# Performance work log

Hardware: AMD Instinct MI355X
Metric: run time of the kernel (lower is better)

## Reference

```python
import jax, jax.numpy as jnp
import numpy as np

HEADS = 4
DIM_HEAD = 32


def setup_inputs() -> dict:
    key = jax.random.key(0)
    k1, k2, k3, k4 = jax.random.split(key, 4)
    dim = 256
    hidden = HEADS * DIM_HEAD  # 128
    x = jax.random.normal(k1, (4, dim, 64, 64), dtype=jnp.float32)
    # 1x1 convs are channel-mixing matmuls; store weights as [out_ch, in_ch]
    w_qkv = jax.random.normal(k2, (3 * hidden, dim), dtype=jnp.float32) * (dim ** -0.5)
    w_out = jax.random.normal(k3, (dim, hidden), dtype=jnp.float32) * (hidden ** -0.5)
    b_out = jax.random.normal(k4, (dim,), dtype=jnp.float32) * 0.02
    return {"x": x, "w_qkv": w_qkv, "w_out": w_out, "b_out": b_out}


def reference(x, w_qkv, w_out, b_out):
    b, c, h, w = x.shape
    n = h * w
    scale = DIM_HEAD ** -0.5
    xf = x.reshape(b, c, n)                                   # b c n
    qkv = jnp.einsum('oc,bcn->bon', w_qkv, xf)                # b (3*H*D) n
    q, k, v = jnp.split(qkv, 3, axis=1)                       # each b (H*D) n
    q = q.reshape(b, HEADS, DIM_HEAD, n) * scale              # b h d n
    k = k.reshape(b, HEADS, DIM_HEAD, n)
    v = v.reshape(b, HEADS, DIM_HEAD, n)
    sim = jnp.einsum('bhdi,bhdj->bhij', q, k)                 # b h n n
    attn = jax.nn.softmax(sim, axis=-1)                       # stable max-subtract inside
    out = jnp.einsum('bhij,bhdj->bhdi', attn, v)              # b h d n
    out = out.reshape(b, HEADS * DIM_HEAD, n)                 # b (h d) n
    out = jnp.einsum('oc,bcn->bon', w_out, out) + b_out[None, :, None]
    return out.reshape(b, -1, h, w)
```

## Files before the change

kernel.cpp:

```cpp
#include <hip/hip_runtime.h>
#include <hip/hip_bf16.h>
#include <stdint.h>

#define B_SZ 4
#define C_IN 256
#define N_SP 4096
#define HEADS 4
#define DH 32
#define HID 128

#define BI 128
#define BJ 64
#define PP 68

typedef short short4v __attribute__((ext_vector_type(4)));
typedef short short8 __attribute__((ext_vector_type(8)));
typedef float f32x4 __attribute__((ext_vector_type(4)));

#if __has_builtin(__builtin_amdgcn_exp2f)
#define EXP2 __builtin_amdgcn_exp2f
#else
#define EXP2 exp2f
#endif

__device__ __forceinline__ short f2bfs(float f) {
  return (short)((__float_as_uint(f) + 0x8000u) >> 16);
}
__device__ __forceinline__ float bfs2f(short s) {
  return __uint_as_float(((uint32_t)(unsigned short)s) << 16);
}
__device__ __forceinline__ uint32_t pk_bf(float a, float b) {
  uint32_t ua = __float_as_uint(a) + 0x8000u;
  uint32_t ub = __float_as_uint(b) + 0x8000u;
  return (ua >> 16) | (ub & 0xffff0000u);
}
__device__ __forceinline__ short8 ld_frag(const short* p) {
  short4v a = *(const short4v*)p;
  short4v b = *(const short4v*)(p + 4);
  return __builtin_shufflevector(a, b, 0, 1, 2, 3, 4, 5, 6, 7);
}
__device__ __forceinline__ f32x4 mfma16(short8 a, short8 b, f32x4 c) {
  return __builtin_amdgcn_mfma_f32_16x16x32_bf16(a, b, c, 0, 0, 0);
}

__global__ __launch_bounds__(256) void prep_k(
    const float* __restrict__ x, const float* __restrict__ w_qkv,
    const float* __restrict__ w_out,
    short* __restrict__ xh, short* __restrict__ xl,
    short* __restrict__ wqh, short* __restrict__ wql,
    short* __restrict__ woh, short* __restrict__ wol) {
  const int t = threadIdx.x;
  const int bx = blockIdx.x;
  if (bx < 256) {
    __shared__ float T[64 * 65];
    const int b = bx >> 6, n0 = (bx & 63) * 64;
    const float* xb = x + (size_t)b * C_IN * N_SP;
    for (int c0 = 0; c0 < C_IN; c0 += 64) {
      {
        const int n = t & 63, cw = t >> 6;
#pragma unroll
        for (int i = 0; i < 16; ++i) {
          const int c = cw * 16 + i;
          T[n * 65 + c] = xb[(size_t)(c0 + c) * N_SP + n0 + n];
        }
      }
      __syncthreads();
      {
        const int n = t >> 2, cg = t & 3;
#pragma unroll
        for (int j = 0; j < 2; ++j) {
          const int c = cg * 16 + j * 8;
          short8 hv, lv;
#pragma unroll
          for (int e = 0; e < 8; ++e) {
            const float v = T[n * 65 + c + e];
            const short hh = f2bfs(v);
            hv[e] = hh;
            lv[e] = f2bfs(v - bfs2f(hh));
          }
          const size_t off = ((size_t)(b * N_SP + n0 + n)) * C_IN + c0 + c;
          *(short8*)(xh + off) = hv;
          *(short8*)(xl + off) = lv;
        }
      }
      __syncthreads();
    }
  } else {
    const int f0 = (bx - 256) * 8192;
#pragma unroll
    for (int j = 0; j < 32; ++j) {
      const int f = f0 + j * 256 + t;
      float v;
      short *dh, *dl;
      int idx;
      if (f < 384 * 256) { v = w_qkv[f]; dh = wqh; dl = wql; idx = f; }
      else { idx = f - 384 * 256; v = w_out[idx]; dh = woh; dl = wol; }
      const short hh = f2bfs(v);
      dh[idx] = hh;
      dl[idx] = f2bfs(v - bfs2f(hh));
    }
  }
}

__global__ __launch_bounds__(256) void qkv_mfma_k(
    const short* __restrict__ xh, const short* __restrict__ xl,
    const short* __restrict__ wqh, const short* __restrict__ wql,
    short* __restrict__ qt, short* __restrict__ kt, short* __restrict__ vt) {
  const int t = threadIdx.x;
  const int lane = t & 63, w = t >> 6;
  const int l15 = lane & 15, quad = lane >> 4;
  const int osec = blockIdx.y, b = blockIdx.z;
  const int n0 = blockIdx.x * 64 + w * 16;
  const size_t xrow = ((size_t)(b * N_SP + n0 + l15)) * C_IN;
  const size_t wrow = ((size_t)(osec * 128 + l15)) * C_IN;
  const bool isv = (osec == 2);
  const f32x4 zz = {0.f, 0.f, 0.f, 0.f};
  f32x4 acc[8];
#pragma unroll
  for (int ot = 0; ot < 8; ++ot) acc[ot] = zz;

  for (int k0 = 0; k0 < C_IN; k0 += 32) {
    const int ko = k0 + quad * 8;
    const short8 xhf = *(const short8*)(xh + xrow + ko);
    const short8 xlf = *(const short8*)(xl + xrow + ko);
#pragma unroll
    for (int ot = 0; ot < 8; ++ot) {
      const size_t wo = wrow + (size_t)ot * 16 * C_IN + ko;
      const short8 whf = *(const short8*)(wqh + wo);
      const short8 wlf = *(const short8*)(wql + wo);
      if (isv) {
        acc[ot] = mfma16(xhf, whf, acc[ot]);
        acc[ot] = mfma16(xlf, whf, acc[ot]);
        acc[ot] = mfma16(xhf, wlf, acc[ot]);
      } else {
        acc[ot] = mfma16(whf, xhf, acc[ot]);
        acc[ot] = mfma16(whf, xlf, acc[ot]);
        acc[ot] = mfma16(wlf, xhf, acc[ot]);
      }
    }
  }

  if (!isv) {
    const float sc = osec ? 1.f : (0.17677669529663687f * 1.4426950408889634f);
    short* dst = osec ? kt : qt;
    const int n = n0 + l15;
#pragma unroll
    for (int ot = 0; ot < 8; ++ot) {
      const int ol = ot * 16 + quad * 4;
      const int h = ol >> 5, d0 = ol & 31;
      short4v p;
#pragma unroll
      for (int r = 0; r < 4; ++r) p[r] = f2bfs(acc[ot][r] * sc);
      *(short4v*)(dst + ((size_t)(b * HEADS + h) * N_SP + n) * DH + d0) = p;
    }
  } else {
    const int n = n0 + quad * 4;
#pragma unroll
    for (int ot = 0; ot < 8; ++ot) {
      const int ol = ot * 16 + l15;
      const int h = ol >> 5, d = ol & 31;
      short4v p;
#pragma unroll
      for (int r = 0; r < 4; ++r) p[r] = f2bfs(acc[ot][r]);
      *(short4v*)(vt + ((size_t)(b * HEADS + h) * DH + d) * N_SP + n) = p;
    }
  }
}

__global__ __launch_bounds__(256, 2) void attn_k(
    const short* __restrict__ qt, const short* __restrict__ kt,
    const short* __restrict__ vt, short* __restrict__ ath,
    short* __restrict__ atl) {
  __shared__ short Ps[BI * PP];
  __shared__ float Osh[DH * 132];
  const int t = threadIdx.x;
  const int lane = t & 63, w = t >> 6;
  const int l15 = lane & 15, quad = lane >> 4;
  const int i0 = blockIdx.x * BI;
  const int bh = blockIdx.y;
  const short* qg = qt + ((size_t)bh * N_SP + i0) * DH;
  const short* kg = kt + (size_t)bh * N_SP * DH;
  const short* vg = vt + (size_t)bh * DH * N_SP;

  short8 bq[2];
#pragma unroll
  for (int tt = 0; tt < 2; ++tt)
    bq[tt] = *(const short8*)(qg + (size_t)(w * 32 + tt * 16 + l15) * DH + quad * 8);

  const f32x4 zz = {0.f, 0.f, 0.f, 0.f};
  f32x4 o_acc[2][2] = {{zz, zz}, {zz, zz}};
  float lsum[2] = {0.f, 0.f};
  short* prow[2];
#pragma unroll
  for (int tt = 0; tt < 2; ++tt) prow[tt] = Ps + (w * 32 + tt * 16 + l15) * PP;

  short8 akA[4], akB[4], vbA[2][2], vbB[2][2];
#pragma unroll
  for (int jt = 0; jt < 4; ++jt)
    akA[jt] = *(const short8*)(kg + (size_t)(jt * 16 + l15) * DH + quad * 8);
#pragma unroll
  for (int dt = 0; dt < 2; ++dt)
#pragma unroll
    for (int kk = 0; kk < 2; ++kk)
      vbA[dt][kk] = *(const short8*)(vg + (size_t)(dt * 16 + l15) * N_SP + kk * 32 + quad * 8);

  auto body = [&](const short8 (&akc)[4], const short8 (&vbc)[2][2],
                  short8 (&akn)[4], short8 (&vbn)[2][2], int jn) {
    f32x4 sf[2][4];
#pragma unroll
    for (int tt = 0; tt < 2; ++tt)
#pragma unroll
      for (int jt = 0; jt < 4; ++jt) sf[tt][jt] = mfma16(akc[jt], bq[tt], zz);
#pragma unroll
    for (int jt = 0; jt < 4; ++jt)
      akn[jt] = *(const short8*)(kg + (size_t)(jn + jt * 16 + l15) * DH + quad * 8);
#pragma unroll
    for (int dt = 0; dt < 2; ++dt)
#pragma unroll
      for (int kk = 0; kk < 2; ++kk)
        vbn[dt][kk] = *(const short8*)(vg + (size_t)(dt * 16 + l15) * N_SP + jn + kk * 32 + quad * 8);
#pragma unroll
    for (int tt = 0; tt < 2; ++tt)
#pragma unroll
      for (int jt = 0; jt < 4; ++jt) {
        const float e0 = EXP2(sf[tt][jt][0]);
        const float e1 = EXP2(sf[tt][jt][1]);
        const float e2 = EXP2(sf[tt][jt][2]);
        const float e3 = EXP2(sf[tt][jt][3]);
        lsum[tt] += (e0 + e1) + (e2 + e3);
        uint2 pk; pk.x = pk_bf(e0, e1); pk.y = pk_bf(e2, e3);
        *(uint2*)(prow[tt] + jt * 16 + quad * 4) = pk;
      }
    asm volatile("s_waitcnt lgkmcnt(0)" ::: "memory");
    short8 pa[2][2];
#pragma unroll
    for (int tt = 0; tt < 2; ++tt)
#pragma unroll
      for (int kk = 0; kk < 2; ++kk) pa[tt][kk] = ld_frag(prow[tt] + kk * 32 + quad * 8);
#pragma unroll
    for (int tt = 0; tt < 2; ++tt)
#pragma unroll
      for (int dt = 0; dt < 2; ++dt) {
        o_acc[tt][dt] = mfma16(pa[tt][0], vbc[dt][0], o_acc[tt][dt]);
        o_acc[tt][dt] = mfma16(pa[tt][1], vbc[dt][1], o_acc[tt][dt]);
      }
  };

  for (int jt0 = 0; jt0 < N_SP; jt0 += 2 * BJ) {
    body(akA, vbA, akB, vbB, (jt0 + BJ) & (N_SP - 1));
    body(akB, vbB, akA, vbA, (jt0 + 2 * BJ) & (N_SP - 1));
  }

#pragma unroll
  for (int tt = 0; tt < 2; ++tt) {
    lsum[tt] += __shfl_xor(lsum[tt], 16);
    lsum[tt] += __shfl_xor(lsum[tt], 32);
  }
  float linv[2][4];
#pragma unroll
  for (int tt = 0; tt < 2; ++tt)
#pragma unroll
    for (int r = 0; r < 4; ++r) linv[tt][r] = 1.f / __shfl(lsum[tt], quad * 4 + r);
#pragma unroll
  for (int tt = 0; tt < 2; ++tt)
#pragma unroll
    for (int dt = 0; dt < 2; ++dt)
#pragma unroll
      for (int r = 0; r < 4; ++r)
        Osh[(dt * 16 + l15) * 132 + w * 32 + tt * 16 + quad * 4 + r] =
            o_acc[tt][dt][r] * linv[tt][r];
  __syncthreads();
  {
    const int ii = t & 127, half = t >> 7;
    const int b = bh >> 2, h = bh & 3;
#pragma unroll
    for (int j = 0; j < 2; ++j) {
      short8 hv, lv;
#pragma unroll
      for (int e = 0; e < 8; ++e) {
        const int d = half * 16 + j * 8 + e;
        const float v = Osh[d * 132 + ii];
        const short hh = f2bfs(v);
        hv[e] = hh;
        lv[e] = f2bfs(v - bfs2f(hh));
      }
      const size_t off =
          ((size_t)(b * N_SP + i0 + ii)) * HID + h * 32 + half * 16 + j * 8;
      *(short8*)(ath + off) = hv;
      *(short8*)(atl + off) = lv;
    }
  }
}

__global__ __launch_bounds__(256) void out_mfma_k(
    const short* __restrict__ ath, const short* __restrict__ atl,
    const short* __restrict__ woh, const short* __restrict__ wol,
    const float* __restrict__ bias, float* __restrict__ out) {
  const int t = threadIdx.x;
  const int lane = t & 63, w = t >> 6;
  const int l15 = lane & 15, quad = lane >> 4;
  const int osec = blockIdx.y, b = blockIdx.z;
  const int n0 = blockIdx.x * 64 + w * 16;
  const size_t arow = ((size_t)(b * N_SP + n0 + l15)) * HID;
  const size_t wrow = ((size_t)(osec * 128 + l15)) * HID;
  const f32x4 zz = {0.f, 0.f, 0.f, 0.f};
  f32x4 acc[8];
#pragma unroll
  for (int ot = 0; ot < 8; ++ot) acc[ot] = zz;

  for (int k0 = 0; k0 < HID; k0 += 32) {
    const int ko = k0 + quad * 8;
    const short8 ahf = *(const short8*)(ath + arow + ko);
    const short8 alf = *(const short8*)(atl + arow + ko);
#pragma unroll
    for (int ot = 0; ot < 8; ++ot) {
      const size_t wo = wrow + (size_t)ot * 16 * HID + ko;
      const short8 whf = *(const short8*)(woh + wo);
      const short8 wlf = *(const short8*)(wol + wo);
      acc[ot] = mfma16(ahf, whf, acc[ot]);
      acc[ot] = mfma16(alf, whf, acc[ot]);
      acc[ot] = mfma16(ahf, wlf, acc[ot]);
    }
  }
#pragma unroll
  for (int ot = 0; ot < 8; ++ot) {
    const int o = osec * 128 + ot * 16 + l15;
    const float bv = bias[o];
    float4 v = make_float4(acc[ot][0] + bv, acc[ot][1] + bv,
                           acc[ot][2] + bv, acc[ot][3] + bv);
    *(float4*)(out + ((size_t)(b * C_IN + o)) * N_SP + n0 + quad * 4) = v;
  }
}

extern "C" void kernel_launch(void* const* d_in, const int* in_sizes, int n_in,
                              void* d_out, int out_size, void* d_ws, size_t ws_size,
                              hipStream_t stream) {
  const float* x = (const float*)d_in[0];
  const float* w_qkv = (const float*)d_in[1];
  const float* w_out = (const float*)d_in[2];
  const float* b_out = (const float*)d_in[3];
  float* out = (float*)d_out;

  short* xh = (short*)d_ws;
  short* xl = xh + (size_t)B_SZ * N_SP * C_IN;
  short* wqh = xl + (size_t)B_SZ * N_SP * C_IN;
  short* wql = wqh + 384 * C_IN;
  short* woh = wql + 384 * C_IN;
  short* wol = woh + C_IN * HID;
  short* qt = wol + C_IN * HID;
  short* kt = qt + (size_t)16 * N_SP * DH;
  short* vt = kt + (size_t)16 * N_SP * DH;
  short* ath = xh;
  short* atl = ath + (size_t)B_SZ * N_SP * HID;

  prep_k<<<dim3(272), 256, 0, stream>>>(x, w_qkv, w_out, xh, xl, wqh, wql, woh, wol);
  qkv_mfma_k<<<dim3(64, 3, B_SZ), 256, 0, stream>>>(xh, xl, wqh, wql, qt, kt, vt);
  attn_k<<<dim3(N_SP / BI, B_SZ * HEADS), 256, 0, stream>>>(qt, kt, vt, ath, atl);
  out_mfma_k<<<dim3(64, 2, B_SZ), 256, 0, stream>>>(ath, atl, woh, wol, b_out, out);
}
```

Baseline: 245.6 us.

## Halve attention query tile, raise occupancy, split prep grid, use hw bf16 pack

The attention kernel now processes 64 query rows per block instead of 128, so each wave handles one 16-row tile, register pressure drops and the launch bound rises to 4 blocks per CU. This gives 1024 attention blocks instead of 512, at the cost of loading every K/V tile twice as often in total. It also replaces the software bf16 packing with the v_cvt_pk_bf16_f32 instruction and wraps the MFMA groups in s_setprio. Separately, the prep kernel is split across channel chunks (1024 blocks instead of 256) to expose more parallelism in the x transpose and conversion.

```diff
diff --git a/kernel.cpp b/kernel.cpp
--- a/kernel.cpp
+++ b/kernel.cpp
@@ -9,7 +9,7 @@
 #define DH 32
 #define HID 128
 
-#define BI 128
+#define BI 64
 #define BJ 64
 #define PP 68
 
@@ -28,11 +28,6 @@
 }
 __device__ __forceinline__ float bfs2f(short s) {
   return __uint_as_float(((uint32_t)(unsigned short)s) << 16);
-}
-__device__ __forceinline__ uint32_t pk_bf(float a, float b) {
-  uint32_t ua = __float_as_uint(a) + 0x8000u;
-  uint32_t ub = __float_as_uint(b) + 0x8000u;
-  return (ua >> 16) | (ub & 0xffff0000u);
 }
 __device__ __forceinline__ short8 ld_frag(const short* p) {
   short4v a = *(const short4v*)p;
@@ -51,42 +46,39 @@
     short* __restrict__ woh, short* __restrict__ wol) {
   const int t = threadIdx.x;
   const int bx = blockIdx.x;
-  if (bx < 256) {
+  if (bx < 1024) {
     __shared__ float T[64 * 65];
-    const int b = bx >> 6, n0 = (bx & 63) * 64;
+    const int b = bx >> 8, n0 = ((bx >> 2) & 63) * 64, c0 = (bx & 3) * 64;
     const float* xb = x + (size_t)b * C_IN * N_SP;
-    for (int c0 = 0; c0 < C_IN; c0 += 64) {
-      {
-        const int n = t & 63, cw = t >> 6;
-#pragma unroll
-        for (int i = 0; i < 16; ++i) {
-          const int c = cw * 16 + i;
-          T[n * 65 + c] = xb[(size_t)(c0 + c) * N_SP + n0 + n];
+    {
+      const int n = t & 63, cw = t >> 6;
+#pragma unroll
+      for (int i = 0; i < 16; ++i) {
+        const int c = cw * 16 + i;
+        T[n * 65 + c] = xb[(size_t)(c0 + c) * N_SP + n0 + n];
+      }
+    }
+    __syncthreads();
+    {
+      const int n = t >> 2, cg = t & 3;
+#pragma unroll
+      for (int j = 0; j < 2; ++j) {
+        const int c = cg * 16 + j * 8;
+        short8 hv, lv;
+#pragma unroll
+        for (int e = 0; e < 8; ++e) {
+          const float v = T[n * 65 + c + e];
+          const short hh = f2bfs(v);
+          hv[e] = hh;
+          lv[e] = f2bfs(v - bfs2f(hh));
         }
+        const size_t off = ((size_t)(b * N_SP + n0 + n)) * C_IN + c0 + c;
+        *(short8*)(xh + off) = hv;
+        *(short8*)(xl + off) = lv;
       }
-      __syncthreads();
-      {
-        const int n = t >> 2, cg = t & 3;
-#pragma unroll
-        for (int j = 0; j < 2; ++j) {
-          const int c = cg * 16 + j * 8;
-          short8 hv, lv;
-#pragma unroll
-          for (int e = 0; e < 8; ++e) {
-            const float v = T[n * 65 + c + e];
-            const short hh = f2bfs(v);
-            hv[e] = hh;
-            lv[e] = f2bfs(v - bfs2f(hh));
-          }
-          const size_t off = ((size_t)(b * N_SP + n0 + n)) * C_IN + c0 + c;
-          *(short8*)(xh + off) = hv;
-          *(short8*)(xl + off) = lv;
-        }
-      }
-      __syncthreads();
     }
   } else {
-    const int f0 = (bx - 256) * 8192;
+    const int f0 = (bx - 1024) * 8192;
 #pragma unroll
     for (int j = 0; j < 32; ++j) {
       const int f = f0 + j * 256 + t;
@@ -167,12 +159,12 @@
   }
 }
 
-__global__ __launch_bounds__(256, 2) void attn_k(
+__global__ __launch_bounds__(256, 4) void attn_k(
     const short* __restrict__ qt, const short* __restrict__ kt,
     const short* __restrict__ vt, short* __restrict__ ath,
     short* __restrict__ atl) {
   __shared__ short Ps[BI * PP];
-  __shared__ float Osh[DH * 132];
+  __shared__ float Osh[DH * 68];
   const int t = threadIdx.x;
   const int lane = t & 63, w = t >> 6;
   const int l15 = lane & 15, quad = lane >> 4;
@@ -182,17 +174,12 @@
   const short* kg = kt + (size_t)bh * N_SP * DH;
   const short* vg = vt + (size_t)bh * DH * N_SP;
 
-  short8 bq[2];
-#pragma unroll
-  for (int tt = 0; tt < 2; ++tt)
-    bq[tt] = *(const short8*)(qg + (size_t)(w * 32 + tt * 16 + l15) * DH + quad * 8);
+  const short8 bq = *(const short8*)(qg + (size_t)(w * 16 + l15) * DH + quad * 8);
 
   const f32x4 zz = {0.f, 0.f, 0.f, 0.f};
-  f32x4 o_acc[2][2] = {{zz, zz}, {zz, zz}};
-  float lsum[2] = {0.f, 0.f};
-  short* prow[2];
-#pragma unroll
-  for (int tt = 0; tt < 2; ++tt) prow[tt] = Ps + (w * 32 + tt * 16 + l15) * PP;
+  f32x4 o_acc[2] = {zz, zz};
+  float lsum = 0.f;
+  short* prow = Ps + (w * 16 + l15) * PP;
 
   short8 akA[4], akB[4], vbA[2][2], vbB[2][2];
 #pragma unroll
@@ -206,11 +193,11 @@
 
   auto body = [&](const short8 (&akc)[4], const short8 (&vbc)[2][2],
                   short8 (&akn)[4], short8 (&vbn)[2][2], int jn) {
-    f32x4 sf[2][4];
-#pragma unroll
-    for (int tt = 0; tt < 2; ++tt)
-#pragma unroll
-      for (int jt = 0; jt < 4; ++jt) sf[tt][jt] = mfma16(akc[jt], bq[tt], zz);
+    f32x4 sf[4];
+    __builtin_amdgcn_s_setprio(1);
+#pragma unroll
+    for (int jt = 0; jt < 4; ++jt) sf[jt] = mfma16(akc[jt], bq, zz);
+    __builtin_amdgcn_s_setprio(0);
 #pragma unroll
     for (int jt = 0; jt < 4; ++jt)
       akn[jt] = *(const short8*)(kg + (size_t)(jn + jt * 16 + l15) * DH + quad * 8);
@@ -220,30 +207,28 @@
       for (int kk = 0; kk < 2; ++kk)
         vbn[dt][kk] = *(const short8*)(vg + (size_t)(dt * 16 + l15) * N_SP + jn + kk * 32 + quad * 8);
 #pragma unroll
-    for (int tt = 0; tt < 2; ++tt)
-#pragma unroll
-      for (int jt = 0; jt < 4; ++jt) {
-        const float e0 = EXP2(sf[tt][jt][0]);
-        const float e1 = EXP2(sf[tt][jt][1]);
-        const float e2 = EXP2(sf[tt][jt][2]);
-        const float e3 = EXP2(sf[tt][jt][3]);
-        lsum[tt] += (e0 + e1) + (e2 + e3);
-        uint2 pk; pk.x = pk_bf(e0, e1); pk.y = pk_bf(e2, e3);
-        *(uint2*)(prow[tt] + jt * 16 + quad * 4) = pk;
-      }
+    for (int jt = 0; jt < 4; ++jt) {
+      const float e0 = EXP2(sf[jt][0]);
+      const float e1 = EXP2(sf[jt][1]);
+      const float e2 = EXP2(sf[jt][2]);
+      const float e3 = EXP2(sf[jt][3]);
+      lsum += (e0 + e1) + (e2 + e3);
+      uint2 pk;
+      asm("v_cvt_pk_bf16_f32 %0, %1, %2" : "=v"(pk.x) : "v"(e0), "v"(e1));
+      asm("v_cvt_pk_bf16_f32 %0, %1, %2" : "=v"(pk.y) : "v"(e2), "v"(e3));
+      *(uint2*)(prow + jt * 16 + quad * 4) = pk;
+    }
     asm volatile("s_waitcnt lgkmcnt(0)" ::: "memory");
-    short8 pa[2][2];
-#pragma unroll
-    for (int tt = 0; tt < 2; ++tt)
-#pragma unroll
-      for (int kk = 0; kk < 2; ++kk) pa[tt][kk] = ld_frag(prow[tt] + kk * 32 + quad * 8);
-#pragma unroll
-    for (int tt = 0; tt < 2; ++tt)
-#pragma unroll
-      for (int dt = 0; dt < 2; ++dt) {
-        o_acc[tt][dt] = mfma16(pa[tt][0], vbc[dt][0], o_acc[tt][dt]);
-        o_acc[tt][dt] = mfma16(pa[tt][1], vbc[dt][1], o_acc[tt][dt]);
-      }
+    short8 pa[2];
+#pragma unroll
+    for (int kk = 0; kk < 2; ++kk) pa[kk] = ld_frag(prow + kk * 32 + quad * 8);
+    __builtin_amdgcn_s_setprio(1);
+#pragma unroll
+    for (int dt = 0; dt < 2; ++dt) {
+      o_acc[dt] = mfma16(pa[0], vbc[dt][0], o_acc[dt]);
+      o_acc[dt] = mfma16(pa[1], vbc[dt][1], o_acc[dt]);
+    }
+    __builtin_amdgcn_s_setprio(0);
   };
 
   for (int jt0 = 0; jt0 < N_SP; jt0 += 2 * BJ) {
@@ -251,44 +236,32 @@
     body(akB, vbB, akA, vbA, (jt0 + 2 * BJ) & (N_SP - 1));
   }
 
-#pragma unroll
-  for (int tt = 0; tt < 2; ++tt) {
-    lsum[tt] += __shfl_xor(lsum[tt], 16);
-    lsum[tt] += __shfl_xor(lsum[tt], 32);
-  }
-  float linv[2][4];
-#pragma unroll
-  for (int tt = 0; tt < 2; ++tt)
-#pragma unroll
-    for (int r = 0; r < 4; ++r) linv[tt][r] = 1.f / __shfl(lsum[tt], quad * 4 + r);
-#pragma unroll
-  for (int tt = 0; tt < 2; ++tt)
-#pragma unroll
-    for (int dt = 0; dt < 2; ++dt)
-#pragma unroll
-      for (int r = 0; r < 4; ++r)
-        Osh[(dt * 16 + l15) * 132 + w * 32 + tt * 16 + quad * 4 + r] =
-            o_acc[tt][dt][r] * linv[tt][r];
+  lsum += __shfl_xor(lsum, 16);
+  lsum += __shfl_xor(lsum, 32);
+  float linv[4];
+#pragma unroll
+  for (int r = 0; r < 4; ++r) linv[r] = 1.f / __shfl(lsum, quad * 4 + r);
+#pragma unroll
+  for (int dt = 0; dt < 2; ++dt)
+#pragma unroll
+    for (int r = 0; r < 4; ++r)
+      Osh[(dt * 16 + l15) * 68 + w * 16 + quad * 4 + r] = o_acc[dt][r] * linv[r];
   __syncthreads();
   {
-    const int ii = t & 127, half = t >> 7;
+    const int ii = t & 63, half = t >> 6;
     const int b = bh >> 2, h = bh & 3;
-#pragma unroll
-    for (int j = 0; j < 2; ++j) {
-      short8 hv, lv;
-#pragma unroll
-      for (int e = 0; e < 8; ++e) {
-        const int d = half * 16 + j * 8 + e;
-        const float v = Osh[d * 132 + ii];
-        const short hh = f2bfs(v);
-        hv[e] = hh;
-        lv[e] = f2bfs(v - bfs2f(hh));
-      }
-      const size_t off =
-          ((size_t)(b * N_SP + i0 + ii)) * HID + h * 32 + half * 16 + j * 8;
-      *(short8*)(ath + off) = hv;
-      *(short8*)(atl + off) = lv;
-    }
+    short8 hv, lv;
+#pragma unroll
+    for (int e = 0; e < 8; ++e) {
+      const int d = half * 8 + e;
+      const float v = Osh[d * 68 + ii];
+      const short hh = f2bfs(v);
+      hv[e] = hh;
+      lv[e] = f2bfs(v - bfs2f(hh));
+    }
+    const size_t off = ((size_t)(b * N_SP + i0 + ii)) * HID + h * 32 + half * 8;
+    *(short8*)(ath + off) = hv;
+    *(short8*)(atl + off) = lv;
   }
 }
 
@@ -353,7 +326,7 @@
   short* ath = xh;
   short* atl = ath + (size_t)B_SZ * N_SP * HID;
 
-  prep_k<<<dim3(272), 256, 0, stream>>>(x, w_qkv, w_out, xh, xl, wqh, wql, woh, wol);
+  prep_k<<<dim3(1040), 256, 0, stream>>>(x, w_qkv, w_out, xh, xl, wqh, wql, woh, wol);
   qkv_mfma_k<<<dim3(64, 3, B_SZ), 256, 0, stream>>>(xh, xl, wqh, wql, qt, kt, vt);
   attn_k<<<dim3(N_SP / BI, B_SZ * HEADS), 256, 0, stream>>>(qt, kt, vt, ath, atl);
   out_mfma_k<<<dim3(64, 2, B_SZ), 256, 0, stream>>>(ath, atl, woh, wol, b_out, out);
```

Result: slower. 329.2 us (+34.0%).
